# Performance work log

Measured on AMD Instinct MI355X. Metric: run time of the kernel, lower is better.

The kernel has to match this reference:

```python
import jax, jax.numpy as jnp
import numpy as np

NUM_LAYERS = 4; HEADS = 8; DIM_HEAD = 64; DIM = 512; FF_INNER = 2048; EPS = 1e-5
B = 32; S = 512
PAGE_VOCAB = 10000; ITEM_VOCAB = 100000; META_VOCAB = 1000
N_WIDE = 8; WIDE_DIM = 64
ATTN_INNER = HEADS * DIM_HEAD
FUSED = ATTN_INNER + DIM_HEAD + DIM_HEAD + 2 * FF_INNER  # q, k, v, swiglu-ff


def rotate_half(x):
    d = x.shape[-1] // 2
    x1, x2 = x[..., :d], x[..., d:]
    return jnp.concatenate([-x2, x1], axis=-1)


def rope_pos(n, d):
    inv_freq = 1.0 / (10000.0 ** (jnp.arange(0, d, 2, dtype=jnp.float32) / d))
    freqs = jnp.arange(n, dtype=jnp.float32)[:, None] * inv_freq[None, :]
    return jnp.concatenate([freqs, freqs], axis=-1)  # (n, d)


def wide_feat(w, bn_g, bn_b, W, bvec):
    # w: (B, n_wide, S); BatchNorm1d eval mode (running mean 0, var 1) -> affine only
    wn = w * (1.0 / np.sqrt(1.0 + EPS)) * bn_g[None, :, None] + bn_b[None, :, None]
    wt = jnp.transpose(wn, (0, 2, 1))  # (B, S, n_wide)
    return jax.nn.leaky_relu(wt @ W + bvec, negative_slope=0.2)


def parallel_block(x, vl, g, Wf, Wa, Wff):
    b, n, _ = x.shape
    mu = x.mean(-1, keepdims=True)
    var = ((x - mu) ** 2).mean(-1, keepdims=True)
    xn = (x - mu) / jnp.sqrt(var + EPS) * g  # gamma-only LayerNorm
    p = xn @ Wf  # (b, n, FUSED)
    q = p[..., :ATTN_INNER]
    k = p[..., ATTN_INNER:ATTN_INNER + DIM_HEAD]
    v = p[..., ATTN_INNER + DIM_HEAD:ATTN_INNER + 2 * DIM_HEAD]
    ff = p[..., ATTN_INNER + 2 * DIM_HEAD:]
    q = jnp.transpose(q.reshape(b, n, HEADS, DIM_HEAD), (0, 2, 1, 3))  # b h n d
    pos = rope_pos(n, DIM_HEAD)
    cos, sin = jnp.cos(pos), jnp.sin(pos)
    q = q * cos + rotate_half(q) * sin
    k = k * cos + rotate_half(k) * sin  # multi-query: k,v shared across heads
    q = q * (DIM_HEAD ** -0.5)
    sim = jnp.einsum('bhid,bjd->bhij', q, k)
    key_pad = jnp.arange(n)[None, :] >= vl[:, None]  # (b, n) True = padded key
    sim = jnp.where(key_pad[:, None, None, :], -jnp.inf, sim)
    attn = jax.nn.softmax(sim, axis=-1)
    out = jnp.einsum('bhij,bjd->bhid', attn, v)
    out = jnp.transpose(out, (0, 2, 1, 3)).reshape(b, n, ATTN_INNER)
    xx, gate = ff[..., :FF_INNER], ff[..., FF_INNER:]
    return out @ Wa + (jax.nn.silu(gate) * xx) @ Wff


def forward(page_in, item_in, item_meta_in, vl_in, page_meta_in,
            page_meta_wide_in, item_meta_wide_in,
            page_emb_table, page_meta_emb_table, item_emb_table,
            item_meta_emb_table, item_pre_emb_table,
            page_wide_W, page_wide_b, page_bn_g, page_bn_b,
            item_wide_W, item_wide_b, item_bn_g, item_bn_b,
            norm_g, fused_W, attn_out_W, ff_out_W):
    page_wide = wide_feat(page_meta_wide_in, page_bn_g, page_bn_b, page_wide_W, page_wide_b)
    item_wide = wide_feat(item_meta_wide_in, item_bn_g, item_bn_b, item_wide_W, item_wide_b)
    page = jnp.concatenate([page_emb_table[page_in], page_meta_emb_table[page_meta_in], page_wide], axis=-1)
    item = jnp.concatenate([item_emb_table[item_in], item_meta_emb_table[item_meta_in],
                            item_pre_emb_table[item_in], item_wide], axis=-1)
    x = page * item  # (B, S, DIM)
    for l in range(NUM_LAYERS):
        x = parallel_block(x, vl_in, norm_g[l], fused_W[l], attn_out_W[l], ff_out_W[l]) + x
    # MeanMaxPooling (dropout=0 in eval)
    return jnp.concatenate([x.mean(axis=1), x.max(axis=1)], axis=-1)  # (B, 2*DIM)


def setup_inputs() -> dict:
    key = jax.random.key(0)
    ks = jax.random.split(key, 24)
    s = 0.02
    return {
        'page_in': jax.random.randint(ks[0], (B, S), 0, PAGE_VOCAB),
        'item_in': jax.random.randint(ks[1], (B, S), 0, ITEM_VOCAB),
        'item_meta_in': jax.random.randint(ks[2], (B, S), 0, META_VOCAB),
        'vl_in': jax.random.randint(ks[3], (B,), 1, S + 1),
        'page_meta_in': jax.random.randint(ks[4], (B, S), 0, META_VOCAB),
        'page_meta_wide_in': jax.random.normal(ks[5], (B, N_WIDE, S), jnp.float32),
        'item_meta_wide_in': jax.random.normal(ks[6], (B, N_WIDE, S), jnp.float32),
        'page_emb_table': jax.random.normal(ks[7], (PAGE_VOCAB, 384), jnp.float32) * s,
        'page_meta_emb_table': jax.random.normal(ks[8], (META_VOCAB, 64), jnp.float32) * s,
        'item_emb_table': jax.random.normal(ks[9], (ITEM_VOCAB, 320), jnp.float32) * s,
        'item_meta_emb_table': jax.random.normal(ks[10], (META_VOCAB, 64), jnp.float32) * s,
        'item_pre_emb_table': jax.random.normal(ks[11], (ITEM_VOCAB, 64), jnp.float32) * s,
        'page_wide_W': jax.random.normal(ks[12], (N_WIDE, WIDE_DIM), jnp.float32) * s,
        'page_wide_b': jnp.zeros((WIDE_DIM,), jnp.float32),
        'page_bn_g': jnp.ones((N_WIDE,), jnp.float32),
        'page_bn_b': jnp.zeros((N_WIDE,), jnp.float32),
        'item_wide_W': jax.random.normal(ks[13], (N_WIDE, WIDE_DIM), jnp.float32) * s,
        'item_wide_b': jnp.zeros((WIDE_DIM,), jnp.float32),
        'item_bn_g': jnp.ones((N_WIDE,), jnp.float32),
        'item_bn_b': jnp.zeros((N_WIDE,), jnp.float32),
        'norm_g': jnp.ones((NUM_LAYERS, DIM), jnp.float32),
        'fused_W': jax.random.normal(ks[14], (NUM_LAYERS, DIM, FUSED), jnp.float32) * s,
        'attn_out_W': jax.random.normal(ks[15], (NUM_LAYERS, ATTN_INNER, DIM), jnp.float32) * s,
        'ff_out_W': jax.random.normal(ks[16], (NUM_LAYERS, FF_INNER, DIM), jnp.float32) * s,
    }


def reference(page_in, item_in, item_meta_in, vl_in, page_meta_in,
              page_meta_wide_in, item_meta_wide_in,
              page_emb_table, page_meta_emb_table, item_emb_table,
              item_meta_emb_table, item_pre_emb_table,
              page_wide_W, page_wide_b, page_bn_g, page_bn_b,
              item_wide_W, item_wide_b, item_bn_g, item_bn_b,
              norm_g, fused_W, attn_out_W, ff_out_W):
    return forward(page_in, item_in, item_meta_in, vl_in, page_meta_in,
                   page_meta_wide_in, item_meta_wide_in,
                   page_emb_table, page_meta_emb_table, item_emb_table,
                   item_meta_emb_table, item_pre_emb_table,
                   page_wide_W, page_wide_b, page_bn_g, page_bn_b,
                   item_wide_W, item_wide_b, item_bn_g, item_bn_b,
                   norm_g, fused_W, attn_out_W, ff_out_W)
```

## Files before the change

### kernel.cpp

```cpp
#include <hip/hip_runtime.h>
#include <math.h>


namespace {
constexpr int SEQ    = 512;
constexpr int NBATCH = 32;
constexpr int DIMM   = 512;
constexpr int NHEAD  = 8;
constexpr int FFIN   = 2048;
constexpr int NFUSED = 4736;
constexpr int NROWS  = NBATCH * SEQ;
constexpr int QKVC   = 640;
}

typedef __bf16 bf16x8 __attribute__((ext_vector_type(8)));
typedef float f32x4 __attribute__((ext_vector_type(4)));
typedef unsigned short ushort8 __attribute__((ext_vector_type(8)));

static __device__ __forceinline__ unsigned short bfhi(float v, float* hf) {
    __bf16 h = (__bf16)v;
    *hf = (float)h;
    return __builtin_bit_cast(unsigned short, h);
}
static __device__ __forceinline__ unsigned short bflo(float v, float hf) {
    __bf16 l = (__bf16)(v - hf);
    return __builtin_bit_cast(unsigned short, l);
}

__global__ __launch_bounds__(512) void build_x_k(
    const int* __restrict__ page_in, const int* __restrict__ item_in,
    const int* __restrict__ item_meta_in, const int* __restrict__ page_meta_in,
    const float* __restrict__ pwide, const float* __restrict__ iwide,
    const float* __restrict__ page_emb, const float* __restrict__ page_meta_emb,
    const float* __restrict__ item_emb, const float* __restrict__ item_meta_emb,
    const float* __restrict__ item_pre_emb,
    const float* __restrict__ pW, const float* __restrict__ pb,
    const float* __restrict__ pg, const float* __restrict__ pbeta,
    const float* __restrict__ iW, const float* __restrict__ ib,
    const float* __restrict__ ig, const float* __restrict__ ibeta,
    float* __restrict__ x)
{
    const int row = blockIdx.x;
    const int b = row >> 9;
    const int s = row & 511;
    const int d = threadIdx.x;
    const float BNS = 0.9999950000374997f;

    float pv, iv;
    if (d < 384) {
        pv = page_emb[(size_t)page_in[row] * 384 + d];
    } else if (d < 448) {
        pv = page_meta_emb[(size_t)page_meta_in[row] * 64 + (d - 384)];
    } else {
        const int dd = d - 448;
        float acc = pb[dd];
        #pragma unroll
        for (int c = 0; c < 8; ++c) {
            float w  = pwide[((size_t)b * 8 + c) * SEQ + s];
            float wn = w * BNS * pg[c] + pbeta[c];
            acc += wn * pW[c * 64 + dd];
        }
        pv = acc > 0.f ? acc : 0.2f * acc;
    }
    if (d < 320) {
        iv = item_emb[(size_t)item_in[row] * 320 + d];
    } else if (d < 384) {
        iv = item_meta_emb[(size_t)item_meta_in[row] * 64 + (d - 320)];
    } else if (d < 448) {
        iv = item_pre_emb[(size_t)item_in[row] * 64 + (d - 384)];
    } else {
        const int dd = d - 448;
        float acc = ib[dd];
        #pragma unroll
        for (int c = 0; c < 8; ++c) {
            float w  = iwide[((size_t)b * 8 + c) * SEQ + s];
            float wn = w * BNS * ig[c] + ibeta[c];
            acc += wn * iW[c * 64 + dd];
        }
        iv = acc > 0.f ? acc : 0.2f * acc;
    }
    x[(size_t)row * DIMM + d] = pv * iv;
}

__global__ __launch_bounds__(256) void trig_k(float* __restrict__ cost,
                                              float* __restrict__ sint)
{
    const int idx = blockIdx.x * 256 + threadIdx.x;
    const int s = idx >> 5, j = idx & 31;
    float invf = powf(10000.0f, -(float)j * (1.0f / 32.0f));
    float ang = (float)s * invf;
    float sn, cs;
    sincosf(ang, &sn, &cs);
    cost[idx] = cs;
    sint[idx] = sn;
}

__global__ __launch_bounds__(256) void ln_k(const float* __restrict__ x,
                                            unsigned short* __restrict__ xnh,
                                            const float* __restrict__ g)
{
    const int row = blockIdx.x;
    const int t = threadIdx.x;
    const float* xr = x + (size_t)row * DIMM;
    __shared__ float red[4];

    float v0 = xr[t], v1 = xr[t + 256];
    float s = v0 + v1;
    #pragma unroll
    for (int o = 32; o; o >>= 1) s += __shfl_xor(s, o);
    if ((t & 63) == 0) red[t >> 6] = s;
    __syncthreads();
    float mu = (red[0] + red[1] + red[2] + red[3]) * (1.0f / 512.0f);
    __syncthreads();

    float d0 = v0 - mu, d1 = v1 - mu;
    float vs = d0 * d0 + d1 * d1;
    #pragma unroll
    for (int o = 32; o; o >>= 1) vs += __shfl_xor(vs, o);
    if ((t & 63) == 0) red[t >> 6] = vs;
    __syncthreads();
    float var = (red[0] + red[1] + red[2] + red[3]) * (1.0f / 512.0f);
    float r = 1.0f / sqrtf(var + 1e-5f);

    const size_t base = (size_t)row * DIMM;
    float o0 = d0 * r * g[t];
    float o1 = d1 * r * g[t + 256];
    float hf;
    xnh[base + t]       = bfhi(o0, &hf);
    xnh[base + t + 256] = bfhi(o1, &hf);
}

template <bool SPLIT>
__global__ __launch_bounds__(256) void wconv_k(const float* __restrict__ W, int ldw,
                                               int col0,
                                               unsigned short* __restrict__ WTh,
                                               unsigned short* __restrict__ WTl,
                                               int ldt)
{
    __shared__ float tile[64][65];
    const int nt = blockIdx.x << 6;
    const int kt = blockIdx.y << 6;
    const int t  = threadIdx.x;

    #pragma unroll
    for (int i = 0; i < 16; ++i) {
        int flat = i * 256 + t;
        int r = flat >> 6, c = flat & 63;
        tile[r][c] = W[(size_t)(kt + r) * ldw + col0 + nt + c];
    }
    __syncthreads();
    #pragma unroll
    for (int i = 0; i < 2; ++i) {
        int flat = i * 256 + t;
        int n = flat >> 3, ck = (flat & 7) << 3;
        ushort8 hv, lv;
        #pragma unroll
        for (int j = 0; j < 8; ++j) {
            float v = tile[ck + j][n];
            float hf;
            hv[j] = bfhi(v, &hf);
            if (SPLIT) lv[j] = bflo(v, hf);
        }
        size_t o = (size_t)(nt + n) * ldt + kt + ck;
        *(ushort8*)&WTh[o] = hv;
        if (SPLIT) *(ushort8*)&WTl[o] = lv;
    }
}

__global__ __launch_bounds__(256) void rope_split_k(
    const float* __restrict__ qkv,
    const float* __restrict__ cost, const float* __restrict__ sint,
    unsigned short* __restrict__ qh,
    unsigned short* __restrict__ kh, unsigned short* __restrict__ kl,
    unsigned short* __restrict__ vT)
{
    const int row = (blockIdx.x << 2) + (threadIdx.x >> 6);
    const int b = row >> 9;
    const int s = row & 511;
    const int d = threadIdx.x & 63;
    const int j = d & 31;

    const float cs = cost[s * 32 + j];
    const float sn = sint[s * 32 + j];

    const float* rowp = qkv + (size_t)row * QKVC;
    const int pair = (d < 32) ? d + 32 : d - 32;
    const float sgn = (d < 32) ? -1.f : 1.f;
    float hf;

    float kv = rowp[512 + d];
    float kp = rowp[512 + pair];
    float kr = kv * cs + sgn * kp * sn;
    size_t kidx = ((size_t)b * 512 + s) * 64 + d;
    kh[kidx] = bfhi(kr, &hf);
    kl[kidx] = bflo(kr, hf);

    float vv = rowp[576 + d];
    vT[((size_t)b * 64 + d) * 512 + s] = bfhi(vv, &hf);

    #pragma unroll
    for (int h = 0; h < NHEAD; ++h) {
        float qv = rowp[h * 64 + d];
        float qp = rowp[h * 64 + pair];
        float qr = (qv * cs + sgn * qp * sn) * 0.125f;
        size_t qidx = (((size_t)b * 8 + h) * 512 + s) * 64 + d;
        qh[qidx] = bfhi(qr, &hf);
    }
}

__global__ __launch_bounds__(256, 4) void mfma_gemm_k(
    const unsigned short* __restrict__ Ah, int lda,
    const unsigned short* __restrict__ BTh, const unsigned short* __restrict__ BTl,
    int ldb, int K,
    float* __restrict__ C, int ldc)
{
    __shared__ unsigned short sA[128 * 64];
    __shared__ unsigned short sBh[64 * 64];
    __shared__ unsigned short sBl[64 * 64];

    const int n0 = blockIdx.x << 6;
    const int m0 = blockIdx.y << 7;
    const int t  = threadIdx.x;
    const int l  = t & 63;
    const int w  = t >> 6;
    const int wm = w >> 1, wn = w & 1;
    const int lr = l & 15, lg = l >> 4;

    f32x4 acc[4][2];
    #pragma unroll
    for (int fm = 0; fm < 4; ++fm)
        #pragma unroll
        for (int fn = 0; fn < 2; ++fn) acc[fm][fn] = (f32x4)0.f;

    for (int k0 = 0; k0 < K; k0 += 64) {
        __syncthreads();
        #pragma unroll
        for (int i = 0; i < 4; ++i) {
            int flat = i * 256 + t;
            int m = flat >> 3, c = flat & 7;
            size_t gidx = (size_t)(m0 + m) * lda + k0 + c * 8;
            int lidx = m * 64 + ((c ^ (m & 7)) << 3);
            *(ushort8*)&sA[lidx] = *(const ushort8*)&Ah[gidx];
        }
        #pragma unroll
        for (int i = 0; i < 2; ++i) {
            int flat = i * 256 + t;
            int n = flat >> 3, c = flat & 7;
            size_t gidx = (size_t)(n0 + n) * ldb + k0 + c * 8;
            int lidx = n * 64 + ((c ^ (n & 7)) << 3);
            *(ushort8*)&sBh[lidx] = *(const ushort8*)&BTh[gidx];
            *(ushort8*)&sBl[lidx] = *(const ushort8*)&BTl[gidx];
        }
        __syncthreads();

        #pragma unroll
        for (int kk = 0; kk < 2; ++kk) {
            const int c = kk * 4 + lg;
            bf16x8 af[4];
            #pragma unroll
            for (int fm = 0; fm < 4; ++fm) {
                int m = wm * 64 + fm * 16 + lr;
                int lidx = m * 64 + ((c ^ (m & 7)) << 3);
                af[fm] = *(bf16x8*)&sA[lidx];
            }
            bf16x8 bh[2], bl[2];
            #pragma unroll
            for (int fn = 0; fn < 2; ++fn) {
                int n = wn * 32 + fn * 16 + lr;
                int lidx = n * 64 + ((c ^ (n & 7)) << 3);
                bh[fn] = *(bf16x8*)&sBh[lidx];
                bl[fn] = *(bf16x8*)&sBl[lidx];
            }
            #pragma unroll
            for (int fm = 0; fm < 4; ++fm)
                #pragma unroll
                for (int fn = 0; fn < 2; ++fn) {
                    acc[fm][fn] = __builtin_amdgcn_mfma_f32_16x16x32_bf16(af[fm], bh[fn], acc[fm][fn], 0, 0, 0);
                    acc[fm][fn] = __builtin_amdgcn_mfma_f32_16x16x32_bf16(af[fm], bl[fn], acc[fm][fn], 0, 0, 0);
                }
        }
    }

    #pragma unroll
    for (int fm = 0; fm < 4; ++fm)
        #pragma unroll
        for (int fn = 0; fn < 2; ++fn) {
            const int n = n0 + wn * 32 + fn * 16 + lr;
            #pragma unroll
            for (int r = 0; r < 4; ++r) {
                const int m = m0 + wm * 64 + fm * 16 + lg * 4 + r;
                C[(size_t)m * ldc + n] = acc[fm][fn][r];
            }
        }
}

__global__ __launch_bounds__(256, 2) void mfma_out_k(
    const unsigned short* __restrict__ A1,
    const unsigned short* __restrict__ B1,
    const unsigned short* __restrict__ A2,
    const unsigned short* __restrict__ B2,
    float* __restrict__ X)
{
    __shared__ unsigned short sA[64 * 64];
    __shared__ unsigned short sB[256 * 64];

    const int n0 = blockIdx.x << 8;
    const int m0 = blockIdx.y << 6;
    const int t  = threadIdx.x;
    const int l  = t & 63;
    const int w  = t >> 6;
    const int lr = l & 15, lg = l >> 4;

    f32x4 acc[4][4];
    #pragma unroll
    for (int fm = 0; fm < 4; ++fm)
        #pragma unroll
        for (int fn = 0; fn < 4; ++fn) acc[fm][fn] = (f32x4)0.f;

    #pragma unroll
    for (int pass = 0; pass < 2; ++pass) {
        const unsigned short* pA = pass ? A2 : A1;
        const unsigned short* pB = pass ? B2 : B1;
        const int lda = pass ? FFIN : DIMM;
        const int KK  = pass ? FFIN : DIMM;

        for (int k0 = 0; k0 < KK; k0 += 64) {
            __syncthreads();
            #pragma unroll
            for (int i = 0; i < 2; ++i) {
                int flat = i * 256 + t;
                int m = flat >> 3, c = flat & 7;
                size_t gidx = (size_t)(m0 + m) * lda + k0 + c * 8;
                int lidx = m * 64 + ((c ^ (m & 7)) << 3);
                *(ushort8*)&sA[lidx] = *(const ushort8*)&pA[gidx];
            }
            #pragma unroll
            for (int i = 0; i < 8; ++i) {
                int flat = i * 256 + t;
                int n = flat >> 3, c = flat & 7;
                size_t gidx = (size_t)(n0 + n) * KK + k0 + c * 8;
                int lidx = n * 64 + ((c ^ (n & 7)) << 3);
                *(ushort8*)&sB[lidx] = *(const ushort8*)&pB[gidx];
            }
            __syncthreads();

            #pragma unroll
            for (int kk = 0; kk < 2; ++kk) {
                const int c = kk * 4 + lg;
                bf16x8 af[4];
                #pragma unroll
                for (int fm = 0; fm < 4; ++fm) {
                    int m = fm * 16 + lr;
                    int lidx = m * 64 + ((c ^ (m & 7)) << 3);
                    af[fm] = *(bf16x8*)&sA[lidx];
                }
                bf16x8 bf[4];
                #pragma unroll
                for (int fn = 0; fn < 4; ++fn) {
                    int n = w * 64 + fn * 16 + lr;
                    int lidx = n * 64 + ((c ^ (n & 7)) << 3);
                    bf[fn] = *(bf16x8*)&sB[lidx];
                }
                #pragma unroll
                for (int fm = 0; fm < 4; ++fm)
                    #pragma unroll
                    for (int fn = 0; fn < 4; ++fn)
                        acc[fm][fn] = __builtin_amdgcn_mfma_f32_16x16x32_bf16(af[fm], bf[fn], acc[fm][fn], 0, 0, 0);
            }
        }
    }

    #pragma unroll
    for (int fm = 0; fm < 4; ++fm)
        #pragma unroll
        for (int fn = 0; fn < 4; ++fn) {
            const int n = n0 + w * 64 + fn * 16 + lr;
            #pragma unroll
            for (int r = 0; r < 4; ++r) {
                const int m = m0 + fm * 16 + lg * 4 + r;
                X[(size_t)m * DIMM + n] += acc[fm][fn][r];
            }
        }
}

__global__ __launch_bounds__(256, 4) void mfma_dual_silu_k(
    const unsigned short* __restrict__ Ah,
    const unsigned short* __restrict__ WTh,
    unsigned short* __restrict__ Hh)
{
    __shared__ unsigned short sA[128 * 64];
    __shared__ unsigned short sBx[64 * 64];
    __shared__ unsigned short sBg[64 * 64];

    const int n0 = blockIdx.x << 6;
    const int m0 = blockIdx.y << 7;
    const int t  = threadIdx.x;
    const int l  = t & 63;
    const int w  = t >> 6;
    const int wm = w >> 1, wn = w & 1;
    const int lr = l & 15, lg = l >> 4;

    f32x4 accX[4][2], accG[4][2];
    #pragma unroll
    for (int fm = 0; fm < 4; ++fm)
        #pragma unroll
        for (int fn = 0; fn < 2; ++fn) {
            accX[fm][fn] = (f32x4)0.f;
            accG[fm][fn] = (f32x4)0.f;
        }

    for (int k0 = 0; k0 < DIMM; k0 += 64) {
        __syncthreads();
        #pragma unroll
        for (int i = 0; i < 4; ++i) {
            int flat = i * 256 + t;
            int m = flat >> 3, c = flat & 7;
            size_t gidx = (size_t)(m0 + m) * DIMM + k0 + c * 8;
            int lidx = m * 64 + ((c ^ (m & 7)) << 3);
            *(ushort8*)&sA[lidx] = *(const ushort8*)&Ah[gidx];
        }
        #pragma unroll
        for (int i = 0; i < 2; ++i) {
            int flat = i * 256 + t;
            int n = flat >> 3, c = flat & 7;
            size_t gx = (size_t)(n0 + n) * DIMM + k0 + c * 8;
            size_t gg = (size_t)(2048 + n0 + n) * DIMM + k0 + c * 8;
            int lidx = n * 64 + ((c ^ (n & 7)) << 3);
            *(ushort8*)&sBx[lidx] = *(const ushort8*)&WTh[gx];
            *(ushort8*)&sBg[lidx] = *(const ushort8*)&WTh[gg];
        }
        __syncthreads();

        #pragma unroll
        for (int kk = 0; kk < 2; ++kk) {
            const int c = kk * 4 + lg;
            bf16x8 af[4];
            #pragma unroll
            for (int fm = 0; fm < 4; ++fm) {
                int m = wm * 64 + fm * 16 + lr;
                int lidx = m * 64 + ((c ^ (m & 7)) << 3);
                af[fm] = *(bf16x8*)&sA[lidx];
            }
            bf16x8 bx[2], bg[2];
            #pragma unroll
            for (int fn = 0; fn < 2; ++fn) {
                int n = wn * 32 + fn * 16 + lr;
                int lidx = n * 64 + ((c ^ (n & 7)) << 3);
                bx[fn] = *(bf16x8*)&sBx[lidx];
                bg[fn] = *(bf16x8*)&sBg[lidx];
            }
            #pragma unroll
            for (int fm = 0; fm < 4; ++fm)
                #pragma unroll
                for (int fn = 0; fn < 2; ++fn) {
                    accX[fm][fn] = __builtin_amdgcn_mfma_f32_16x16x32_bf16(af[fm], bx[fn], accX[fm][fn], 0, 0, 0);
                    accG[fm][fn] = __builtin_amdgcn_mfma_f32_16x16x32_bf16(af[fm], bg[fn], accG[fm][fn], 0, 0, 0);
                }
        }
    }

    __syncthreads();
    #pragma unroll
    for (int fm = 0; fm < 4; ++fm)
        #pragma unroll
        for (int fn = 0; fn < 2; ++fn) {
            const int nl = wn * 32 + fn * 16 + lr;
            const int cc = nl >> 3;
            #pragma unroll
            for (int r = 0; r < 4; ++r) {
                const int ml = wm * 64 + fm * 16 + lg * 4 + r;
                float gv = accG[fm][fn][r];
                float xv = accX[fm][fn][r];
                float sig = 1.0f / (1.0f + __expf(-gv));
                float hv = gv * sig * xv;
                float hf;
                sA[ml * 64 + ((cc ^ (ml & 7)) << 3) + (nl & 7)] = bfhi(hv, &hf);
            }
        }
    __syncthreads();
    #pragma unroll
    for (int i = 0; i < 4; ++i) {
        int flat = i * 256 + t;
        int m = flat >> 3, c = flat & 7;
        ushort8 v = *(ushort8*)&sA[m * 64 + ((c ^ (m & 7)) << 3)];
        __builtin_nontemporal_store(v, (ushort8*)&Hh[(size_t)(m0 + m) * FFIN + n0 + c * 8]);
    }
}

__global__ __launch_bounds__(256) void attn_mfma_k(
    const unsigned short* __restrict__ qh,
    const unsigned short* __restrict__ kh, const unsigned short* __restrict__ kl,
    const unsigned short* __restrict__ vT,
    unsigned short* __restrict__ ctxh,
    const int* __restrict__ vl)
{
    __shared__ unsigned short sKh[64 * 64];
    __shared__ unsigned short sKl[64 * 64];
    __shared__ unsigned short sVT[64 * 64];
    __shared__ unsigned short sP[64 * 64];

    const int i0 = blockIdx.x << 6;
    const int h  = blockIdx.y;
    const int b  = blockIdx.z;
    const int t  = threadIdx.x;
    const int l  = t & 63;
    const int w  = t >> 6;
    const int lr = l & 15, lg = l >> 4;
    const int VL = vl[b];
    const int ntiles = (VL + 63) >> 6;

    bf16x8 qfh[2];
    {
        size_t base = (((size_t)(b * 8 + h) * 512) + i0 + w * 16 + lr) * 64 + lg * 8;
        qfh[0] = *(const bf16x8*)&qh[base];
        qfh[1] = *(const bf16x8*)&qh[base + 32];
    }

    float mrow[4], lrow[4];
    f32x4 oacc[4];
    #pragma unroll
    for (int r = 0; r < 4; ++r) { mrow[r] = -3.0e38f; lrow[r] = 0.f; }
    #pragma unroll
    for (int nb = 0; nb < 4; ++nb) oacc[nb] = (f32x4)0.f;

    for (int jt = 0; jt < ntiles; ++jt) {
        const int j0 = jt << 6;
        __syncthreads();
        #pragma unroll
        for (int i = 0; i < 2; ++i) {
            int flat = i * 256 + t;
            int m = flat >> 3, c = flat & 7;
            int lidx = m * 64 + ((c ^ (m & 7)) << 3);
            size_t kg = ((size_t)b * 512 + j0 + m) * 64 + c * 8;
            *(ushort8*)&sKh[lidx] = *(const ushort8*)&kh[kg];
            *(ushort8*)&sKl[lidx] = *(const ushort8*)&kl[kg];
            size_t vg = ((size_t)b * 64 + m) * 512 + j0 + c * 8;
            *(ushort8*)&sVT[lidx] = *(const ushort8*)&vT[vg];
        }
        __syncthreads();

        f32x4 accS[4];
        #pragma unroll
        for (int nb = 0; nb < 4; ++nb) accS[nb] = (f32x4)0.f;
        #pragma unroll
        for (int ks = 0; ks < 2; ++ks) {
            const int c = ks * 4 + lg;
            #pragma unroll
            for (int nb = 0; nb < 4; ++nb) {
                int n = nb * 16 + lr;
                int lidx = n * 64 + ((c ^ (n & 7)) << 3);
                bf16x8 kfh = *(bf16x8*)&sKh[lidx];
                bf16x8 kfl = *(bf16x8*)&sKl[lidx];
                accS[nb] = __builtin_amdgcn_mfma_f32_16x16x32_bf16(qfh[ks], kfh, accS[nb], 0, 0, 0);
                accS[nb] = __builtin_amdgcn_mfma_f32_16x16x32_bf16(qfh[ks], kfl, accS[nb], 0, 0, 0);
            }
        }

        #pragma unroll
        for (int nb = 0; nb < 4; ++nb) {
            if (j0 + nb * 16 + lr >= VL) {
                #pragma unroll
                for (int r = 0; r < 4; ++r) accS[nb][r] = -3.0e38f;
            }
        }

        #pragma unroll
        for (int r = 0; r < 4; ++r) {
            float rm = fmaxf(fmaxf(accS[0][r], accS[1][r]), fmaxf(accS[2][r], accS[3][r]));
            #pragma unroll
            for (int off = 8; off; off >>= 1) rm = fmaxf(rm, __shfl_xor(rm, off));
            float nm = fmaxf(mrow[r], rm);
            float scl = __expf(mrow[r] - nm);
            mrow[r] = nm;
            float ps = 0.f;
            #pragma unroll
            for (int nb = 0; nb < 4; ++nb) {
                float p = __expf(accS[nb][r] - nm);
                accS[nb][r] = p;
                ps += p;
            }
            lrow[r] = lrow[r] * scl + ps;
            #pragma unroll
            for (int nb = 0; nb < 4; ++nb) oacc[nb][r] *= scl;
        }

        #pragma unroll
        for (int nb = 0; nb < 4; ++nb) {
            int cc = nb * 2 + (lr >> 3);
            #pragma unroll
            for (int r = 0; r < 4; ++r) {
                int q = w * 16 + lg * 4 + r;
                int lidx = q * 64 + ((cc ^ (q & 7)) << 3) + (lr & 7);
                float hf2;
                sP[lidx] = bfhi(accS[nb][r], &hf2);
            }
        }

        #pragma unroll
        for (int ks = 0; ks < 2; ++ks) {
            const int c = ks * 4 + lg;
            int qrow = w * 16 + lr;
            int plidx = qrow * 64 + ((c ^ (qrow & 7)) << 3);
            bf16x8 pf = *(bf16x8*)&sP[plidx];
            #pragma unroll
            for (int nb = 0; nb < 4; ++nb) {
                int n = nb * 16 + lr;
                int lidx = n * 64 + ((c ^ (n & 7)) << 3);
                bf16x8 vf = *(bf16x8*)&sVT[lidx];
                oacc[nb] = __builtin_amdgcn_mfma_f32_16x16x32_bf16(pf, vf, oacc[nb], 0, 0, 0);
            }
        }
    }

    #pragma unroll
    for (int r = 0; r < 4; ++r) {
        float lt = lrow[r];
        #pragma unroll
        for (int off = 8; off; off >>= 1) lt += __shfl_xor(lt, off);
        float inv = 1.0f / lt;
        const int row = (b << 9) + i0 + w * 16 + lg * 4 + r;
        const size_t base = (size_t)row * DIMM + h * 64;
        #pragma unroll
        for (int nb = 0; nb < 4; ++nb) {
            float v = oacc[nb][r] * inv;
            float hf;
            ctxh[base + nb * 16 + lr] = bfhi(v, &hf);
        }
    }
}

__global__ __launch_bounds__(512) void pool_part_k(const float* __restrict__ x,
                                                   float* __restrict__ psum,
                                                   float* __restrict__ pmax)
{
    const int seg = blockIdx.x;
    const int b   = blockIdx.y;
    const int d   = threadIdx.x;
    const float* xb = x + ((size_t)(b << 9) + (seg << 6)) * DIMM;
    float s = 0.f, m = -3.0e38f;
    for (int i = 0; i < 64; ++i) {
        float v = xb[(size_t)i * DIMM + d];
        s += v;
        m = fmaxf(m, v);
    }
    psum[((size_t)b * 8 + seg) * DIMM + d] = s;
    pmax[((size_t)b * 8 + seg) * DIMM + d] = m;
}

__global__ __launch_bounds__(512) void pool_comb_k(const float* __restrict__ psum,
                                                   const float* __restrict__ pmax,
                                                   float* __restrict__ out)
{
    const int b = blockIdx.x;
    const int d = threadIdx.x;
    float s = 0.f, m = -3.0e38f;
    #pragma unroll
    for (int seg = 0; seg < 8; ++seg) {
        s += psum[((size_t)b * 8 + seg) * DIMM + d];
        m = fmaxf(m, pmax[((size_t)b * 8 + seg) * DIMM + d]);
    }
    out[b * 1024 + d] = s * (1.0f / 512.0f);
    out[b * 1024 + 512 + d] = m;
}

extern "C" void kernel_launch(void* const* d_in, const int* in_sizes, int n_in,
                              void* d_out, int out_size, void* d_ws, size_t ws_size,
                              hipStream_t stream)
{
    const int*   page_in        = (const int*)d_in[0];
    const int*   item_in        = (const int*)d_in[1];
    const int*   item_meta_in   = (const int*)d_in[2];
    const int*   vl_in          = (const int*)d_in[3];
    const int*   page_meta_in   = (const int*)d_in[4];
    const float* pwide          = (const float*)d_in[5];
    const float* iwide          = (const float*)d_in[6];
    const float* page_emb       = (const float*)d_in[7];
    const float* page_meta_emb  = (const float*)d_in[8];
    const float* item_emb       = (const float*)d_in[9];
    const float* item_meta_emb  = (const float*)d_in[10];
    const float* item_pre_emb   = (const float*)d_in[11];
    const float* pW             = (const float*)d_in[12];
    const float* pb             = (const float*)d_in[13];
    const float* pg             = (const float*)d_in[14];
    const float* pbeta          = (const float*)d_in[15];
    const float* iW             = (const float*)d_in[16];
    const float* ib             = (const float*)d_in[17];
    const float* ig             = (const float*)d_in[18];
    const float* ibeta          = (const float*)d_in[19];
    const float* norm_g         = (const float*)d_in[20];
    const float* fused_W        = (const float*)d_in[21];
    const float* attn_out_W     = (const float*)d_in[22];
    const float* ff_out_W       = (const float*)d_in[23];
    float* out = (float*)d_out;

    float* ws  = (float*)d_ws;
    float* x    = ws;
    unsigned short* xnh = (unsigned short*)(x + (size_t)NROWS * DIMM);
    unsigned short* qhb = xnh + (size_t)NROWS * DIMM;
    float* qkv = (float*)(qhb + (size_t)NROWS * DIMM);
    unsigned short* hh   = (unsigned short*)(qkv + (size_t)NROWS * QKVC);
    unsigned short* ctxh = hh + (size_t)NROWS * FFIN;
    float* psum = (float*)(ctxh + (size_t)NROWS * DIMM);
    float* pmax = psum + (size_t)NBATCH * 8 * DIMM;
    unsigned short* WqTh = (unsigned short*)(pmax + (size_t)NBATCH * 8 * DIMM);
    unsigned short* WqTl = WqTh + (size_t)QKVC * DIMM;
    unsigned short* WdTh = WqTl + (size_t)QKVC * DIMM;
    unsigned short* WaTh = WdTh + (size_t)4096 * DIMM;
    unsigned short* WfTh = WaTh + (size_t)DIMM * DIMM;
    unsigned short* khb  = WfTh + (size_t)DIMM * FFIN;
    unsigned short* klb  = khb + (size_t)NBATCH * SEQ * 64;
    unsigned short* vTb  = klb + (size_t)NBATCH * SEQ * 64;
    float* cost = (float*)(vTb + (size_t)NBATCH * 64 * SEQ);
    float* sint = cost + 512 * 32;

    build_x_k<<<NROWS, 512, 0, stream>>>(
        page_in, item_in, item_meta_in, page_meta_in, pwide, iwide,
        page_emb, page_meta_emb, item_emb, item_meta_emb, item_pre_emb,
        pW, pb, pg, pbeta, iW, ib, ig, ibeta, x);

    trig_k<<<64, 256, 0, stream>>>(cost, sint);

    for (int l = 0; l < 4; ++l) {
        const float* Wf  = fused_W    + (size_t)l * DIMM * NFUSED;
        const float* Wa  = attn_out_W + (size_t)l * DIMM * DIMM;
        const float* Wff = ff_out_W   + (size_t)l * FFIN * DIMM;
        const float* g   = norm_g     + (size_t)l * DIMM;

        ln_k<<<NROWS, 256, 0, stream>>>(x, xnh, g);

        wconv_k<true><<<dim3(QKVC / 64, DIMM / 64), 256, 0, stream>>>(
            Wf, NFUSED, 0, WqTh, WqTl, DIMM);
        wconv_k<false><<<dim3(4096 / 64, DIMM / 64), 256, 0, stream>>>(
            Wf, NFUSED, 640, WdTh, nullptr, DIMM);
        wconv_k<false><<<dim3(DIMM / 64, DIMM / 64), 256, 0, stream>>>(
            Wa, DIMM, 0, WaTh, nullptr, DIMM);
        wconv_k<false><<<dim3(DIMM / 64, FFIN / 64), 256, 0, stream>>>(
            Wff, DIMM, 0, WfTh, nullptr, FFIN);

        mfma_gemm_k<<<dim3(QKVC / 64, NROWS / 128), 256, 0, stream>>>(
            xnh, DIMM, WqTh, WqTl, DIMM, DIMM, qkv, QKVC);

        mfma_dual_silu_k<<<dim3(FFIN / 64, NROWS / 128), 256, 0, stream>>>(
            xnh, WdTh, hh);

        rope_split_k<<<NROWS / 4, 256, 0, stream>>>(
            qkv, cost, sint, qhb, khb, klb, vTb);

        attn_mfma_k<<<dim3(SEQ / 64, NHEAD, NBATCH), 256, 0, stream>>>(
            qhb, khb, klb, vTb, ctxh, vl_in);

        mfma_out_k<<<dim3(2, NROWS / 64), 256, 0, stream>>>(
            ctxh, WaTh, hh, WfTh, x);
    }

    pool_part_k<<<dim3(8, NBATCH), 512, 0, stream>>>(x, psum, pmax);
    pool_comb_k<<<NBATCH, 512, 0, stream>>>(psum, pmax, out);
}
```

Measured before the change: 1.074 ms.

## Fuse RoPE and q/k/v split into the QKV projection GEMM epilogue

The QKV GEMM no longer writes an fp32 qkv buffer. Its epilogue stages the accumulator tile in shared memory with a rotated layout, then applies RoPE and writes bf16 q, split hi/lo k, and transposed v straight from there. This removes the separate rope_split_k launch and the fp32 round trip of the 16384x640 intermediate. In exchange the GEMM gains an extra shared-memory stage and two barriers, and each block's epilogue branches on its column tile.

```diff
diff --git a/kernel.cpp b/kernel.cpp
--- a/kernel.cpp
+++ b/kernel.cpp
@@ -167,56 +167,19 @@
     }
 }
 
-__global__ __launch_bounds__(256) void rope_split_k(
-    const float* __restrict__ qkv,
+__global__ __launch_bounds__(256, 4) void mfma_qkv_rope_k(
+    const unsigned short* __restrict__ Ah,
+    const unsigned short* __restrict__ BTh, const unsigned short* __restrict__ BTl,
     const float* __restrict__ cost, const float* __restrict__ sint,
     unsigned short* __restrict__ qh,
     unsigned short* __restrict__ kh, unsigned short* __restrict__ kl,
     unsigned short* __restrict__ vT)
 {
-    const int row = (blockIdx.x << 2) + (threadIdx.x >> 6);
-    const int b = row >> 9;
-    const int s = row & 511;
-    const int d = threadIdx.x & 63;
-    const int j = d & 31;
-
-    const float cs = cost[s * 32 + j];
-    const float sn = sint[s * 32 + j];
-
-    const float* rowp = qkv + (size_t)row * QKVC;
-    const int pair = (d < 32) ? d + 32 : d - 32;
-    const float sgn = (d < 32) ? -1.f : 1.f;
-    float hf;
-
-    float kv = rowp[512 + d];
-    float kp = rowp[512 + pair];
-    float kr = kv * cs + sgn * kp * sn;
-    size_t kidx = ((size_t)b * 512 + s) * 64 + d;
-    kh[kidx] = bfhi(kr, &hf);
-    kl[kidx] = bflo(kr, hf);
-
-    float vv = rowp[576 + d];
-    vT[((size_t)b * 64 + d) * 512 + s] = bfhi(vv, &hf);
-
-    #pragma unroll
-    for (int h = 0; h < NHEAD; ++h) {
-        float qv = rowp[h * 64 + d];
-        float qp = rowp[h * 64 + pair];
-        float qr = (qv * cs + sgn * qp * sn) * 0.125f;
-        size_t qidx = (((size_t)b * 8 + h) * 512 + s) * 64 + d;
-        qh[qidx] = bfhi(qr, &hf);
-    }
-}
-
-__global__ __launch_bounds__(256, 4) void mfma_gemm_k(
-    const unsigned short* __restrict__ Ah, int lda,
-    const unsigned short* __restrict__ BTh, const unsigned short* __restrict__ BTl,
-    int ldb, int K,
-    float* __restrict__ C, int ldc)
-{
-    __shared__ unsigned short sA[128 * 64];
-    __shared__ unsigned short sBh[64 * 64];
-    __shared__ unsigned short sBl[64 * 64];
+    __shared__ unsigned short smem[128 * 64 + 64 * 64 + 64 * 64];
+    unsigned short* sA  = smem;
+    unsigned short* sBh = smem + 128 * 64;
+    unsigned short* sBl = smem + 128 * 64 + 64 * 64;
+    float* tileF = (float*)smem;
 
     const int n0 = blockIdx.x << 6;
     const int m0 = blockIdx.y << 7;
@@ -232,13 +195,13 @@
         #pragma unroll
         for (int fn = 0; fn < 2; ++fn) acc[fm][fn] = (f32x4)0.f;
 
-    for (int k0 = 0; k0 < K; k0 += 64) {
+    for (int k0 = 0; k0 < DIMM; k0 += 64) {
         __syncthreads();
         #pragma unroll
         for (int i = 0; i < 4; ++i) {
             int flat = i * 256 + t;
             int m = flat >> 3, c = flat & 7;
-            size_t gidx = (size_t)(m0 + m) * lda + k0 + c * 8;
+            size_t gidx = (size_t)(m0 + m) * DIMM + k0 + c * 8;
             int lidx = m * 64 + ((c ^ (m & 7)) << 3);
             *(ushort8*)&sA[lidx] = *(const ushort8*)&Ah[gidx];
         }
@@ -246,7 +209,7 @@
         for (int i = 0; i < 2; ++i) {
             int flat = i * 256 + t;
             int n = flat >> 3, c = flat & 7;
-            size_t gidx = (size_t)(n0 + n) * ldb + k0 + c * 8;
+            size_t gidx = (size_t)(n0 + n) * DIMM + k0 + c * 8;
             int lidx = n * 64 + ((c ^ (n & 7)) << 3);
             *(ushort8*)&sBh[lidx] = *(const ushort8*)&BTh[gidx];
             *(ushort8*)&sBl[lidx] = *(const ushort8*)&BTl[gidx];
@@ -281,17 +244,66 @@
         }
     }
 
+    __syncthreads();
     #pragma unroll
     for (int fm = 0; fm < 4; ++fm)
         #pragma unroll
         for (int fn = 0; fn < 2; ++fn) {
-            const int n = n0 + wn * 32 + fn * 16 + lr;
+            const int nl = wn * 32 + fn * 16 + lr;
             #pragma unroll
             for (int r = 0; r < 4; ++r) {
-                const int m = m0 + wm * 64 + fm * 16 + lg * 4 + r;
-                C[(size_t)m * ldc + n] = acc[fm][fn][r];
-            }
-        }
+                const int ml = wm * 64 + fm * 16 + lg * 4 + r;
+                tileF[ml * 64 + ((nl + ml) & 63)] = acc[fm][fn][r];
+            }
+        }
+    __syncthreads();
+
+    const int tid = n0 >> 6;
+    const int gb  = m0 >> 9;
+    const int sb  = m0 & 511;
+
+    if (tid < 8) {
+        #pragma unroll 4
+        for (int i = 0; i < 32; ++i) {
+            int flat = i * 256 + t;
+            int d = flat & 63, sl = flat >> 6;
+            int s = sb + sl;
+            float v  = tileF[sl * 64 + ((d + sl) & 63)];
+            float vp = tileF[sl * 64 + (((d ^ 32) + sl) & 63)];
+            float cs = cost[s * 32 + (d & 31)];
+            float sn = sint[s * 32 + (d & 31)];
+            float sgn = (d < 32) ? -1.f : 1.f;
+            float o = (v * cs + sgn * vp * sn) * 0.125f;
+            float hf;
+            qh[(((size_t)gb * 8 + tid) * 512 + s) * 64 + d] = bfhi(o, &hf);
+        }
+    } else if (tid == 8) {
+        #pragma unroll 4
+        for (int i = 0; i < 32; ++i) {
+            int flat = i * 256 + t;
+            int d = flat & 63, sl = flat >> 6;
+            int s = sb + sl;
+            float v  = tileF[sl * 64 + ((d + sl) & 63)];
+            float vp = tileF[sl * 64 + (((d ^ 32) + sl) & 63)];
+            float cs = cost[s * 32 + (d & 31)];
+            float sn = sint[s * 32 + (d & 31)];
+            float sgn = (d < 32) ? -1.f : 1.f;
+            float o = v * cs + sgn * vp * sn;
+            float hf;
+            size_t idx = ((size_t)gb * 512 + s) * 64 + d;
+            kh[idx] = bfhi(o, &hf);
+            kl[idx] = bflo(o, hf);
+        }
+    } else {
+        #pragma unroll 4
+        for (int i = 0; i < 32; ++i) {
+            int flat = i * 256 + t;
+            int sl = flat & 127, d = flat >> 7;
+            float v = tileF[sl * 64 + ((d + sl) & 63)];
+            float hf;
+            vT[((size_t)gb * 64 + d) * 512 + sb + sl] = bfhi(v, &hf);
+        }
+    }
 }
 
 __global__ __launch_bounds__(256, 2) void mfma_out_k(
@@ -697,8 +709,7 @@
     float* x    = ws;
     unsigned short* xnh = (unsigned short*)(x + (size_t)NROWS * DIMM);
     unsigned short* qhb = xnh + (size_t)NROWS * DIMM;
-    float* qkv = (float*)(qhb + (size_t)NROWS * DIMM);
-    unsigned short* hh   = (unsigned short*)(qkv + (size_t)NROWS * QKVC);
+    unsigned short* hh   = qhb + (size_t)NROWS * DIMM;
     unsigned short* ctxh = hh + (size_t)NROWS * FFIN;
     float* psum = (float*)(ctxh + (size_t)NROWS * DIMM);
     float* pmax = psum + (size_t)NBATCH * 8 * DIMM;
@@ -737,15 +748,12 @@
         wconv_k<false><<<dim3(DIMM / 64, FFIN / 64), 256, 0, stream>>>(
             Wff, DIMM, 0, WfTh, nullptr, FFIN);
 
-        mfma_gemm_k<<<dim3(QKVC / 64, NROWS / 128), 256, 0, stream>>>(
-            xnh, DIMM, WqTh, WqTl, DIMM, DIMM, qkv, QKVC);
+        mfma_qkv_rope_k<<<dim3(QKVC / 64, NROWS / 128), 256, 0, stream>>>(
+            xnh, WqTh, WqTl, cost, sint, qhb, khb, klb, vTb);
 
         mfma_dual_silu_k<<<dim3(FFIN / 64, NROWS / 128), 256, 0, stream>>>(
             xnh, WdTh, hh);
 
-        rope_split_k<<<NROWS / 4, 256, 0, stream>>>(
-            qkv, cost, sint, qhb, khb, klb, vTb);
-
         attn_mfma_k<<<dim3(SEQ / 64, NHEAD, NBATCH), 256, 0, stream>>>(
             qhb, khb, klb, vTb, ctxh, vl_in);
 
```

After: 1.014 ms (median of 2 runs). -5.6%, faster.
